# Kernel optimization log

Hardware: AMD Instinct MI355X
Metric: run time of the kernel (lower is better)

Reference implementation:

```python
import jax, jax.numpy as jnp
import numpy as np

K_CORR = 2048        # num_correspondences (init kwarg)
MAX_CORR = 8192      # static pad size for the variable-length nonzero output
THRES_START = 0.5
THRES_STEP = 0.01


def setup_inputs() -> dict:
    key = jax.random.key(0)
    k1, k2, k3 = jax.random.split(key, 3)
    N = M = 8193  # 8192 superpoints + 1 dustbin
    # shift so exp(scores) is mostly well below the 0.5 starting threshold,
    # making the iterative threshold search actually iterate (as in practice
    # with log-domain OT scores)
    matching_scores = jax.random.normal(k1, (N, M), dtype=jnp.float32) - 5.0
    ref_n2p_scores_c = jax.random.uniform(k2, (N - 1,), dtype=jnp.float32)
    src_n2p_scores_c = jax.random.uniform(k3, (M - 1,), dtype=jnp.float32)
    return {
        "matching_scores": matching_scores,
        "ref_n2p_scores_c": ref_n2p_scores_c,
        "src_n2p_scores_c": src_n2p_scores_c,
    }


def _find_thres(inner, k):
    """Replicates: while count(score[:-1,:-1] > thres) < k: thres -= 0.01."""
    def cond(t):
        return jnp.sum(inner > t) < k
    def body(t):
        return t - jnp.float32(THRES_STEP)
    return jax.lax.while_loop(cond, body, jnp.float32(THRES_START))


def reference(matching_scores, ref_n2p_scores_c, src_n2p_scores_c):
    s = jnp.exp(matching_scores)
    # n2p reweighting of the non-dustbin block, as in the torch in-place update
    inner = s[:-1, :-1] * (ref_n2p_scores_c[:, None] * src_n2p_scores_c[None, :])
    # threshold search is discrete -> not differentiated
    thres = _find_thres(jax.lax.stop_gradient(inner), K_CORR)
    mask = inner > thres
    count = jnp.sum(mask)
    # torch returns variable-length nonzero in row-major order; we pad to MAX_CORR
    r, c = jnp.nonzero(mask, size=MAX_CORR, fill_value=0)
    valid = jnp.arange(MAX_CORR) < count
    corr_scores = jnp.where(valid, inner[r, c], 0.0)
    ref_corr_indices = jnp.where(valid, r, -1)
    src_corr_indices = jnp.where(valid, c, -1)
    return ref_corr_indices, src_corr_indices, corr_scores
```

## Files before the change

### kernel.cpp

```cpp
#include <hip/hip_runtime.h>

#define NROWS 8192
#define NCOLS 8192
#define LD    8193
#define NBINS 64
#define KCORR 2048
#define MAXC  8192
#define CAP   192
#define RPB   4
#define FCUT_LOG (-2.5257286443082556f)

__device__ __forceinline__ float inner_val(float m, float rr, float sc) {
    float p = rr * sc;
    return expf(m) * p;
}

__global__ void init_kernel(float* __restrict__ out, unsigned* __restrict__ hist,
                            unsigned* __restrict__ ovfl) {
    int i = blockIdx.x * blockDim.x + threadIdx.x;
    if (i < 2 * MAXC)       out[i] = -1.0f;
    else if (i < 3 * MAXC)  out[i] = 0.0f;
    if (i < NBINS) hist[i] = 0u;
    if (i == NBINS) *ovfl = 0u;
}

__global__ __launch_bounds__(256) void hist_kernel(
    const float* __restrict__ ms, const float* __restrict__ refs,
    const float* __restrict__ srcs, unsigned* __restrict__ hist,
    unsigned* __restrict__ candcnt, unsigned* __restrict__ cand_col,
    float* __restrict__ cand_v, unsigned* __restrict__ ovfl, int use_cand)
{
    __shared__ float t[NBINS];
    __shared__ unsigned sub[NBINS];
    __shared__ unsigned cnt[RPB];
    __shared__ uint2 pairs[RPB * CAP];
    int tid = threadIdx.x;
    if (tid == 0) {
        float tv = 0.5f;
        for (int n = 0; n < NBINS; ++n) { t[n] = tv; tv = tv - 0.01f; }
    }
    if (tid < NBINS) sub[tid] = 0u;
    if (tid < RPB) cnt[tid] = 0u;
    __syncthreads();

    int r0 = blockIdx.x * RPB;

    auto push = [&](int r, int col, float m) {
        unsigned slot = atomicAdd(&cnt[r], 1u);
        if (slot < CAP)
            pairs[r * CAP + slot] = make_uint2((unsigned)col, __float_as_uint(m));
    };
    auto issue = [&](int b, float4* dst) {
        int r = b >> 1, h = b & 1;
        int row = r0 + r;
        int s = (4 - (row & 3)) & 3;
        const float4* p4 = (const float4*)(ms + (size_t)row * LD + s);
        int nb = (NCOLS - s) >> 2;
        #pragma unroll
        for (int k = 0; k < 4; ++k) {
            int i = h * 1024 + k * 256 + tid;
            if ((h == 1 && k == 3) ? (i < nb) : true) dst[k] = p4[i];
            else dst[k] = make_float4(-1e30f, -1e30f, -1e30f, -1e30f);
        }
    };
    auto consume = [&](int b, const float4* src4) {
        int r = b >> 1, h = b & 1;
        int s = (4 - ((r0 + r) & 3)) & 3;
        #pragma unroll
        for (int k = 0; k < 4; ++k) {
            float4 q = src4[k];
            int c0 = s + 4 * (h * 1024 + k * 256 + tid);
            bool a0 = q.x > FCUT_LOG, a1 = q.y > FCUT_LOG;
            bool a2 = q.z > FCUT_LOG, a3 = q.w > FCUT_LOG;
            if (a0 | a1 | a2 | a3) {
                if (a0) push(r, c0 + 0, q.x);
                if (a1) push(r, c0 + 1, q.y);
                if (a2) push(r, c0 + 2, q.z);
                if (a3) push(r, c0 + 3, q.w);
            }
        }
    };

    float4 buf[2][4];
    issue(0, buf[0]);
    #pragma unroll
    for (int b = 0; b < 2 * RPB; ++b) {
        if (b + 1 < 2 * RPB) issue(b + 1, buf[(b + 1) & 1]);
        consume(b, buf[b & 1]);
    }

    if (tid < RPB * 8) {
        int r = tid >> 3, e = tid & 7;
        int row = r0 + r;
        int s = (4 - (row & 3)) & 3;
        int nb = (NCOLS - s) >> 2;
        int done = s + 4 * nb;
        int col = -1;
        if (e < s) col = e;
        else if (e - s < NCOLS - done) col = done + (e - s);
        if (col >= 0) {
            float m = ms[(size_t)row * LD + col];
            if (m > FCUT_LOG) push(r, col, m);
        }
    }
    __syncthreads();

    for (int r = 0; r < RPB; ++r) {
        int row = r0 + r;
        unsigned C = cnt[r];
        unsigned Cc = (C < CAP) ? C : CAP;
        float rr = refs[row];
        for (unsigned i = tid; i < Cc; i += 256) {
            uint2 pr = pairs[r * CAP + i];
            int col = (int)pr.x;
            float m = __uint_as_float(pr.y);
            float v = inner_val(m, rr, srcs[col]);
            int g = (int)floorf((0.5f - v) * 100.0f) + 1;
            g = (g < 0) ? 0 : ((g > NBINS) ? NBINS : g);
            while (g < NBINS && t[g] >= v) ++g;
            while (g > 0 && t[g - 1] < v) --g;
            atomicAdd(&sub[g], 1u);
            if (use_cand) {
                cand_col[(size_t)row * CAP + i] = (unsigned)col;
                cand_v[(size_t)row * CAP + i]   = v;
            }
        }
        if (tid == 0) {
            if (use_cand) candcnt[row] = C;
            if (C > CAP) atomicOr(ovfl, 1u);
        }
    }
    __syncthreads();

    if (tid < 64) {
        unsigned v = sub[tid];
        unsigned p = v;
        #pragma unroll
        for (int off = 1; off < 64; off <<= 1) {
            unsigned u = __shfl_up(p, off);
            if (tid >= off) p += u;
        }
        unsigned binned = __shfl(p, 63);
        unsigned g = (tid == 63) ? (v + (unsigned)(RPB * NCOLS) - binned) : v;
        if (g) atomicAdd(&hist[tid], g);
    }
}

__global__ void mid_kernel(const unsigned* __restrict__ hist,
                           float* __restrict__ thres, unsigned* __restrict__ nstar) {
    int tid = threadIdx.x;
    if (tid < 64) {
        unsigned h = hist[tid];
        unsigned cum = h;
        #pragma unroll
        for (int off = 1; off < 64; off <<= 1) {
            unsigned u = __shfl_up(cum, off);
            if (tid >= off) cum += u;
        }
        unsigned long long mk = __ballot(cum >= (unsigned)KCORR);
        int nsel = mk ? (int)(__ffsll((unsigned long long)mk) - 1) : (NBINS - 1);
        if (tid == 0) {
            float tv = 0.5f;
            for (int n = 0; n < nsel; ++n) tv = tv - 0.01f;
            *thres = tv;
            *nstar = (unsigned)nsel;
        }
    }
}

__global__ __launch_bounds__(256) void rowcnt_kernel(
    const float* __restrict__ ms, const float* __restrict__ refs,
    const float* __restrict__ srcs, const float* __restrict__ thresp,
    const unsigned* __restrict__ nstar, const unsigned* __restrict__ ovfl,
    const unsigned* __restrict__ candcnt, const float* __restrict__ cand_v,
    unsigned* __restrict__ rowcnt, int use_cand)
{
    int ns = (int)*nstar;
    if (!(use_cand && ns <= 41 && *ovfl == 0u)) return;
    int tid = threadIdx.x, wv = tid >> 6, lane = tid & 63;
    int row = blockIdx.x * 4 + wv;
    float th = *thresp;
    unsigned C = candcnt[row];
    unsigned c = 0;
    if (C <= CAP) {
        const float* cv = cand_v + (size_t)row * CAP;
        for (unsigned i = lane; i < C; i += 64)
            c += (cv[i] > th) ? 1u : 0u;
    } else {
        float rr = refs[row];
        const float* mrow = ms + (size_t)row * LD;
        for (int col = lane; col < NCOLS; col += 64)
            c += (inner_val(mrow[col], rr, srcs[col]) > th) ? 1u : 0u;
    }
    #pragma unroll
    for (int off = 32; off > 0; off >>= 1) c += __shfl_down(c, off);
    if (lane == 0) rowcnt[row] = c;
}

__global__ __launch_bounds__(256) void count2_kernel(
    const float* __restrict__ ms, const float* __restrict__ refs,
    const float* __restrict__ srcs, const float* __restrict__ thresp,
    const unsigned* __restrict__ nstar, const unsigned* __restrict__ ovfl,
    unsigned* __restrict__ rowcnt, int use_cand)
{
    int ns = (int)*nstar;
    if (use_cand && ns <= 41 && *ovfl == 0u) return;
    __shared__ unsigned tot;
    float th = *thresp;
    for (int r4 = 0; r4 < 4; ++r4) {
        int row = blockIdx.x * 4 + r4;
        if (threadIdx.x == 0) tot = 0;
        __syncthreads();
        float rr = refs[row];
        const float* mrow = ms + (size_t)row * LD;
        unsigned c = 0;
        for (int col = threadIdx.x; col < NCOLS; col += 256)
            c += (inner_val(mrow[col], rr, srcs[col]) > th) ? 1u : 0u;
        atomicAdd(&tot, c);
        __syncthreads();
        if (threadIdx.x == 0) rowcnt[row] = tot;
        __syncthreads();
    }
}

__global__ __launch_bounds__(1024) void scan_kernel(
    const unsigned* __restrict__ rowcnt, unsigned* __restrict__ rowoff)
{
    __shared__ unsigned ssum[1024];
    int tid = threadIdx.x;
    int r0 = tid * 8;
    unsigned c[8], s = 0;
    #pragma unroll
    for (int k = 0; k < 8; ++k) { c[k] = rowcnt[r0 + k]; s += c[k]; }
    ssum[tid] = s;
    __syncthreads();
    for (int off = 1; off < 1024; off <<= 1) {
        unsigned v = (tid >= off) ? ssum[tid - off] : 0u;
        __syncthreads();
        ssum[tid] += v;
        __syncthreads();
    }
    unsigned excl = ssum[tid] - s;
    #pragma unroll
    for (int k = 0; k < 8; ++k) { rowoff[r0 + k] = excl; excl += c[k]; }
    if (tid == 1023) rowoff[NROWS] = excl;
}

__global__ __launch_bounds__(256) void cwrite_kernel(
    const float* __restrict__ ms, const float* __restrict__ refs,
    const float* __restrict__ srcs, const float* __restrict__ thresp,
    const unsigned* __restrict__ nstar, const unsigned* __restrict__ ovfl,
    const unsigned* __restrict__ rowoff, const unsigned* __restrict__ candcnt,
    const unsigned* __restrict__ cand_col, const float* __restrict__ cand_v,
    float* __restrict__ out, int use_cand)
{
    __shared__ unsigned s_col[4][64];
    __shared__ float    s_val[4][64];
    int tid = threadIdx.x, wv = tid >> 6, lane = tid & 63;
    int row = blockIdx.x * 4 + wv;
    unsigned base = rowoff[row], next = rowoff[row + 1];
    if (base == next || base >= MAXC) return;
    float th = *thresp;
    int ns = (int)*nstar;
    unsigned k = next - base;
    bool full = (!use_cand) || (ns >= 42) || (*ovfl != 0u) ||
                (candcnt[row] > CAP) || (k > 64);

    if (!full) {
        unsigned C = candcnt[row];
        const unsigned* cc = cand_col + (size_t)row * CAP;
        const float*    cv = cand_v  + (size_t)row * CAP;
        unsigned nrun = 0;
        for (unsigned c0 = 0; c0 < C; c0 += 64) {
            unsigned i = c0 + lane;
            bool sel = false; unsigned col = 0; float v = 0.f;
            if (i < C) { col = cc[i]; v = cv[i]; sel = (v > th); }
            unsigned long long mk = __ballot(sel);
            if (sel) {
                unsigned idx = nrun + (unsigned)__popcll(mk & ((1ull << lane) - 1ull));
                if (idx < 64) { s_col[wv][idx] = col; s_val[wv][idx] = v; }
            }
            nrun += (unsigned)__popcll(mk);
        }
        __builtin_amdgcn_s_waitcnt(0);
        __builtin_amdgcn_wave_barrier();
        unsigned kk = (nrun < k) ? nrun : k;
        if (kk > 64) kk = 64;
        if (lane < (int)kk) {
            unsigned mycol = s_col[wv][lane];
            float    myval = s_val[wv][lane];
            unsigned rank = 0;
            for (unsigned j = 0; j < kk; ++j)
                rank += (s_col[wv][j] < mycol) ? 1u : 0u;
            unsigned pos = base + rank;
            if (pos < MAXC) {
                out[pos]            = (float)row;
                out[MAXC + pos]     = (float)mycol;
                out[2 * MAXC + pos] = myval;
            }
        }
        return;
    }

    float rr = refs[row];
    const float* mrow = ms + (size_t)row * LD;
    unsigned running = base;
    for (int c0 = 0; c0 < NCOLS && running < next && running < MAXC; c0 += 64) {
        int col = c0 + lane;
        float v = inner_val(mrow[col], rr, srcs[col]);
        bool pred = v > th;
        unsigned long long mk = __ballot(pred);
        if (pred) {
            unsigned pos = running + (unsigned)__popcll(mk & ((1ull << lane) - 1ull));
            if (pos < MAXC) {
                out[pos]            = (float)row;
                out[MAXC + pos]     = (float)col;
                out[2 * MAXC + pos] = v;
            }
        }
        running += (unsigned)__popcll(mk);
    }
}

extern "C" void kernel_launch(void* const* d_in, const int* in_sizes, int n_in,
                              void* d_out, int out_size, void* d_ws, size_t ws_size,
                              hipStream_t stream) {
    const float* ms  = (const float*)d_in[0];
    const float* ref = (const float*)d_in[1];
    const float* src = (const float*)d_in[2];
    float* out = (float*)d_out;

    char* w = (char*)d_ws;
    unsigned* hist   = (unsigned*)(w);
    float*    thres  = (float*)(w + 256);
    unsigned* nstar  = (unsigned*)(w + 260);
    unsigned* ovfl   = (unsigned*)(w + 264);
    unsigned* rowcnt = (unsigned*)(w + 512);
    unsigned* rowoff = (unsigned*)(w + 512 + NROWS * 4);
    size_t cc_off = 512 + (size_t)NROWS * 4 + (size_t)(NROWS + 1) * 4;
    cc_off = (cc_off + 255) & ~(size_t)255;
    unsigned* candcnt  = (unsigned*)(w + cc_off);
    size_t col_off = cc_off + (size_t)NROWS * 4;
    unsigned* cand_col = (unsigned*)(w + col_off);
    size_t cv_off = col_off + (size_t)NROWS * CAP * 4;
    float* cand_v      = (float*)(w + cv_off);
    size_t end_off = cv_off + (size_t)NROWS * CAP * 4;

    int use_cand = (ws_size >= end_off) ? 1 : 0;

    init_kernel<<<96, 256, 0, stream>>>(out, hist, ovfl);
    hist_kernel<<<NROWS / RPB, 256, 0, stream>>>(ms, ref, src, hist, candcnt,
                                                 cand_col, cand_v, ovfl, use_cand);
    mid_kernel<<<1, 64, 0, stream>>>(hist, thres, nstar);
    rowcnt_kernel<<<NROWS / 4, 256, 0, stream>>>(ms, ref, src, thres, nstar,
                                                 ovfl, candcnt, cand_v, rowcnt,
                                                 use_cand);
    count2_kernel<<<NROWS / 4, 256, 0, stream>>>(ms, ref, src, thres, nstar,
                                                 ovfl, rowcnt, use_cand);
    scan_kernel<<<1, 1024, 0, stream>>>(rowcnt, rowoff);
    cwrite_kernel<<<NROWS / 4, 256, 0, stream>>>(ms, ref, src, thres, nstar,
                                                 ovfl, rowoff, candcnt, cand_col,
                                                 cand_v, out, use_cand);
}
```

Before: 382.7 us.

## Split histogram pass into flat mask scan plus sparse candidate expansion

Replaces the row-blocked histogram kernel with a flat, grid-strided float4 scan over the whole matrix. That scan emits 64-bit ballot masks of quads holding a value above the log cutoff. A second kernel expands only the flagged quads, bins them, and appends candidates per row with global atomics. A separate full-matrix histogram fallback (fb_hist plus mid2) runs only when the cutoff-based histogram cannot reach K. The aim is perfectly coalesced, alignment-free streaming of the large input and less per-row shared-memory work, at the cost of an extra mask buffer, global atomics on candcnt, and integer divisions to recover row and column.

Result: slower. 431.0 us (+12.6%).

```diff
diff --git a/kernel.cpp b/kernel.cpp
--- a/kernel.cpp
+++ b/kernel.cpp
@@ -2,181 +2,226 @@
 
 #define NROWS 8192
 #define NCOLS 8192
-#define LD    8193
+#define LDIM  8193
 #define NBINS 64
 #define KCORR 2048
 #define MAXC  8192
 #define CAP   192
-#define RPB   4
 #define FCUT_LOG (-2.5257286443082556f)
+
+#define NQUAD   16781312
+#define TILEQ   1024
+#define NTILES  16388
+#define NGROUPS 262208
 
 __device__ __forceinline__ float inner_val(float m, float rr, float sc) {
     float p = rr * sc;
     return expf(m) * p;
 }
 
+__device__ __forceinline__ void fold_thresholds(float* t) {
+    float tv = 0.5f;
+    for (int n = 0; n < NBINS; ++n) { t[n] = tv; tv = tv - 0.01f; }
+}
+
+__device__ __forceinline__ int exact_bin(float v, const float* t) {
+    int g = (int)floorf((0.5f - v) * 100.0f) + 1;
+    g = (g < 0) ? 0 : ((g > NBINS) ? NBINS : g);
+    while (g < NBINS && t[g] >= v) ++g;
+    while (g > 0 && t[g - 1] < v) --g;
+    return (g > 63) ? 63 : g;
+}
+
 __global__ void init_kernel(float* __restrict__ out, unsigned* __restrict__ hist,
-                            unsigned* __restrict__ ovfl) {
+                            unsigned* __restrict__ hist2,
+                            unsigned* __restrict__ candcnt,
+                            unsigned* __restrict__ fullmode) {
     int i = blockIdx.x * blockDim.x + threadIdx.x;
     if (i < 2 * MAXC)       out[i] = -1.0f;
     else if (i < 3 * MAXC)  out[i] = 0.0f;
-    if (i < NBINS) hist[i] = 0u;
-    if (i == NBINS) *ovfl = 0u;
-}
-
-__global__ __launch_bounds__(256) void hist_kernel(
+    if (i < NBINS) { hist[i] = 0u; hist2[i] = 0u; }
+    if (i == NBINS) *fullmode = 0u;
+    if (i < NROWS) candcnt[i] = 0u;
+}
+
+__global__ __launch_bounds__(256) void scan_mask_kernel(
+    const float* __restrict__ ms, unsigned long long* __restrict__ masks)
+{
+    const int tid = threadIdx.x;
+    const int lane = tid & 63, wv = tid >> 6;
+    const float4* m4 = (const float4*)ms;
+    const int g = gridDim.x;
+
+    float4 b0[4], b1[4];
+    auto issue = [&](int t, float4* B) {
+        const float4* p = m4 + (size_t)t * TILEQ + tid;
+        #pragma unroll
+        for (int k = 0; k < 4; ++k) B[k] = p[k * 256];
+    };
+    auto emit = [&](int t, const float4* B) {
+        unsigned long long mk0 = __ballot((B[0].x > FCUT_LOG) | (B[0].y > FCUT_LOG) |
+                                          (B[0].z > FCUT_LOG) | (B[0].w > FCUT_LOG));
+        unsigned long long mk1 = __ballot((B[1].x > FCUT_LOG) | (B[1].y > FCUT_LOG) |
+                                          (B[1].z > FCUT_LOG) | (B[1].w > FCUT_LOG));
+        unsigned long long mk2 = __ballot((B[2].x > FCUT_LOG) | (B[2].y > FCUT_LOG) |
+                                          (B[2].z > FCUT_LOG) | (B[2].w > FCUT_LOG));
+        unsigned long long mk3 = __ballot((B[3].x > FCUT_LOG) | (B[3].y > FCUT_LOG) |
+                                          (B[3].z > FCUT_LOG) | (B[3].w > FCUT_LOG));
+        unsigned long long val = (lane & 2) ? ((lane & 1) ? mk3 : mk2)
+                                            : ((lane & 1) ? mk1 : mk0);
+        if (lane < 4)
+            masks[(size_t)t * 16 + wv * 4 + lane] = val;
+    };
+
+    int t = blockIdx.x;
+    issue(t, b0);
+    while (true) {
+        int t1 = t + g;
+        if (t1 < NTILES) issue(t1, b1);
+        emit(t, b0);
+        t = t1;
+        if (t >= NTILES) break;
+        int t2 = t + g;
+        if (t2 < NTILES) issue(t2, b0);
+        emit(t, b1);
+        t = t2;
+        if (t >= NTILES) break;
+    }
+}
+
+__global__ __launch_bounds__(256) void expand_kernel(
     const float* __restrict__ ms, const float* __restrict__ refs,
-    const float* __restrict__ srcs, unsigned* __restrict__ hist,
-    unsigned* __restrict__ candcnt, unsigned* __restrict__ cand_col,
-    float* __restrict__ cand_v, unsigned* __restrict__ ovfl, int use_cand)
+    const float* __restrict__ srcs, const unsigned long long* __restrict__ masks,
+    unsigned* __restrict__ hist, unsigned* __restrict__ candcnt,
+    unsigned* __restrict__ cand_col, float* __restrict__ cand_v, int use_cand)
 {
     __shared__ float t[NBINS];
     __shared__ unsigned sub[NBINS];
-    __shared__ unsigned cnt[RPB];
-    __shared__ uint2 pairs[RPB * CAP];
     int tid = threadIdx.x;
+    if (tid == 0) fold_thresholds(t);
+    if (tid < NBINS) sub[tid] = 0u;
+    __syncthreads();
+
+    for (int i = blockIdx.x * 256 + tid; i < NGROUPS; i += gridDim.x * 256) {
+        unsigned long long mask = masks[i];
+        if (!mask) continue;
+        int tile = i >> 4, r = i & 15, w = r >> 2, k = r & 3;
+        int quadBase = tile * TILEQ + k * 256 + w * 64;
+        while (mask) {
+            int b = __ffsll((long long)mask) - 1;
+            mask &= mask - 1;
+            int q = quadBase + b;
+            float4 v4 = ((const float4*)ms)[q];
+            int e0 = q * 4;
+            #pragma unroll
+            for (int j = 0; j < 4; ++j) {
+                float m = (j == 0) ? v4.x : (j == 1) ? v4.y : (j == 2) ? v4.z : v4.w;
+                if (!(m > FCUT_LOG)) continue;
+                unsigned e = (unsigned)(e0 + j);
+                unsigned row = e / 8193u;
+                unsigned col = e - row * 8193u;
+                if (row >= NROWS || col >= NCOLS) continue;
+                float v = inner_val(m, refs[row], srcs[col]);
+                atomicAdd(&sub[exact_bin(v, t)], 1u);
+                if (use_cand) {
+                    unsigned slot = atomicAdd(&candcnt[row], 1u);
+                    if (slot < CAP) {
+                        cand_col[(size_t)row * CAP + slot] = col;
+                        cand_v[(size_t)row * CAP + slot]   = v;
+                    }
+                }
+            }
+        }
+    }
+    __syncthreads();
+    if (tid < NBINS && sub[tid]) atomicAdd(&hist[tid], sub[tid]);
+}
+
+__global__ void mid_kernel(const unsigned* __restrict__ hist,
+                           float* __restrict__ thres, unsigned* __restrict__ nstar,
+                           unsigned* __restrict__ fullmode) {
+    int tid = threadIdx.x;
+    unsigned cum = hist[tid];
+    #pragma unroll
+    for (int off = 1; off < 64; off <<= 1) {
+        unsigned u = __shfl_up(cum, off);
+        if (tid >= off) cum += u;
+    }
+    unsigned long long mk = __ballot(cum >= (unsigned)KCORR);
     if (tid == 0) {
-        float tv = 0.5f;
-        for (int n = 0; n < NBINS; ++n) { t[n] = tv; tv = tv - 0.01f; }
-    }
-    if (tid < NBINS) sub[tid] = 0u;
-    if (tid < RPB) cnt[tid] = 0u;
-    __syncthreads();
-
-    int r0 = blockIdx.x * RPB;
-
-    auto push = [&](int r, int col, float m) {
-        unsigned slot = atomicAdd(&cnt[r], 1u);
-        if (slot < CAP)
-            pairs[r * CAP + slot] = make_uint2((unsigned)col, __float_as_uint(m));
-    };
-    auto issue = [&](int b, float4* dst) {
-        int r = b >> 1, h = b & 1;
-        int row = r0 + r;
-        int s = (4 - (row & 3)) & 3;
-        const float4* p4 = (const float4*)(ms + (size_t)row * LD + s);
-        int nb = (NCOLS - s) >> 2;
-        #pragma unroll
-        for (int k = 0; k < 4; ++k) {
-            int i = h * 1024 + k * 256 + tid;
-            if ((h == 1 && k == 3) ? (i < nb) : true) dst[k] = p4[i];
-            else dst[k] = make_float4(-1e30f, -1e30f, -1e30f, -1e30f);
-        }
-    };
-    auto consume = [&](int b, const float4* src4) {
-        int r = b >> 1, h = b & 1;
-        int s = (4 - ((r0 + r) & 3)) & 3;
-        #pragma unroll
-        for (int k = 0; k < 4; ++k) {
-            float4 q = src4[k];
-            int c0 = s + 4 * (h * 1024 + k * 256 + tid);
-            bool a0 = q.x > FCUT_LOG, a1 = q.y > FCUT_LOG;
-            bool a2 = q.z > FCUT_LOG, a3 = q.w > FCUT_LOG;
-            if (a0 | a1 | a2 | a3) {
-                if (a0) push(r, c0 + 0, q.x);
-                if (a1) push(r, c0 + 1, q.y);
-                if (a2) push(r, c0 + 2, q.z);
-                if (a3) push(r, c0 + 3, q.w);
-            }
-        }
-    };
-
-    float4 buf[2][4];
-    issue(0, buf[0]);
-    #pragma unroll
-    for (int b = 0; b < 2 * RPB; ++b) {
-        if (b + 1 < 2 * RPB) issue(b + 1, buf[(b + 1) & 1]);
-        consume(b, buf[b & 1]);
-    }
-
-    if (tid < RPB * 8) {
-        int r = tid >> 3, e = tid & 7;
-        int row = r0 + r;
-        int s = (4 - (row & 3)) & 3;
-        int nb = (NCOLS - s) >> 2;
-        int done = s + 4 * nb;
-        int col = -1;
-        if (e < s) col = e;
-        else if (e - s < NCOLS - done) col = done + (e - s);
-        if (col >= 0) {
-            float m = ms[(size_t)row * LD + col];
-            if (m > FCUT_LOG) push(r, col, m);
-        }
-    }
-    __syncthreads();
-
-    for (int r = 0; r < RPB; ++r) {
-        int row = r0 + r;
-        unsigned C = cnt[r];
-        unsigned Cc = (C < CAP) ? C : CAP;
-        float rr = refs[row];
-        for (unsigned i = tid; i < Cc; i += 256) {
-            uint2 pr = pairs[r * CAP + i];
-            int col = (int)pr.x;
-            float m = __uint_as_float(pr.y);
-            float v = inner_val(m, rr, srcs[col]);
-            int g = (int)floorf((0.5f - v) * 100.0f) + 1;
-            g = (g < 0) ? 0 : ((g > NBINS) ? NBINS : g);
-            while (g < NBINS && t[g] >= v) ++g;
-            while (g > 0 && t[g - 1] < v) --g;
-            atomicAdd(&sub[g], 1u);
-            if (use_cand) {
-                cand_col[(size_t)row * CAP + i] = (unsigned)col;
-                cand_v[(size_t)row * CAP + i]   = v;
-            }
-        }
-        if (tid == 0) {
-            if (use_cand) candcnt[row] = C;
-            if (C > CAP) atomicOr(ovfl, 1u);
-        }
-    }
-    __syncthreads();
-
-    if (tid < 64) {
-        unsigned v = sub[tid];
-        unsigned p = v;
-        #pragma unroll
-        for (int off = 1; off < 64; off <<= 1) {
-            unsigned u = __shfl_up(p, off);
-            if (tid >= off) p += u;
-        }
-        unsigned binned = __shfl(p, 63);
-        unsigned g = (tid == 63) ? (v + (unsigned)(RPB * NCOLS) - binned) : v;
-        if (g) atomicAdd(&hist[tid], g);
-    }
-}
-
-__global__ void mid_kernel(const unsigned* __restrict__ hist,
-                           float* __restrict__ thres, unsigned* __restrict__ nstar) {
-    int tid = threadIdx.x;
-    if (tid < 64) {
-        unsigned h = hist[tid];
-        unsigned cum = h;
-        #pragma unroll
-        for (int off = 1; off < 64; off <<= 1) {
-            unsigned u = __shfl_up(cum, off);
-            if (tid >= off) cum += u;
-        }
-        unsigned long long mk = __ballot(cum >= (unsigned)KCORR);
-        int nsel = mk ? (int)(__ffsll((unsigned long long)mk) - 1) : (NBINS - 1);
-        if (tid == 0) {
+        int nsel = mk ? (int)(__ffsll((long long)mk) - 1) : NBINS;
+        if (nsel <= 41) {
             float tv = 0.5f;
             for (int n = 0; n < nsel; ++n) tv = tv - 0.01f;
-            *thres = tv;
-            *nstar = (unsigned)nsel;
-        }
+            *thres = tv; *nstar = (unsigned)nsel; *fullmode = 0u;
+        } else {
+            *fullmode = 1u; *nstar = 63u; *thres = -1e30f;
+        }
+    }
+}
+
+__global__ __launch_bounds__(256) void fb_hist_kernel(
+    const float* __restrict__ ms, const float* __restrict__ refs,
+    const float* __restrict__ srcs, const unsigned* __restrict__ fullmode,
+    unsigned* __restrict__ hist2)
+{
+    if (*fullmode == 0u) return;
+    __shared__ float t[NBINS];
+    __shared__ unsigned sub[64 * 65];
+    int tid = threadIdx.x, lane = tid & 63;
+    if (tid == 0) fold_thresholds(t);
+    for (int i = tid; i < 64 * 65; i += 256) sub[i] = 0u;
+    __syncthreads();
+    unsigned* mysub = sub + lane * 65;
+    for (int q = blockIdx.x * 256 + tid; q < NQUAD; q += gridDim.x * 256) {
+        float4 v4 = ((const float4*)ms)[q];
+        int e0 = q * 4;
+        #pragma unroll
+        for (int j = 0; j < 4; ++j) {
+            float m = (j == 0) ? v4.x : (j == 1) ? v4.y : (j == 2) ? v4.z : v4.w;
+            unsigned e = (unsigned)(e0 + j);
+            unsigned row = e / 8193u;
+            unsigned col = e - row * 8193u;
+            if (row >= NROWS || col >= NCOLS) continue;
+            float v = inner_val(m, refs[row], srcs[col]);
+            atomicAdd(&mysub[exact_bin(v, t)], 1u);
+        }
+    }
+    __syncthreads();
+    if (tid < 64) {
+        unsigned s = 0;
+        for (int c = 0; c < 64; ++c) s += sub[c * 65 + tid];
+        if (s) atomicAdd(&hist2[tid], s);
+    }
+}
+
+__global__ void mid2_kernel(const unsigned* __restrict__ hist2,
+                            const unsigned* __restrict__ fullmode,
+                            float* __restrict__ thres, unsigned* __restrict__ nstar) {
+    if (*fullmode == 0u) return;
+    int tid = threadIdx.x;
+    unsigned cum = hist2[tid];
+    #pragma unroll
+    for (int off = 1; off < 64; off <<= 1) {
+        unsigned u = __shfl_up(cum, off);
+        if (tid >= off) cum += u;
+    }
+    unsigned long long mk = __ballot(cum >= (unsigned)KCORR);
+    if (tid == 0) {
+        int nsel = mk ? (int)(__ffsll((long long)mk) - 1) : (NBINS - 1);
+        float tv = 0.5f;
+        for (int n = 0; n < nsel; ++n) tv = tv - 0.01f;
+        *thres = tv; *nstar = (unsigned)nsel;
     }
 }
 
 __global__ __launch_bounds__(256) void rowcnt_kernel(
     const float* __restrict__ ms, const float* __restrict__ refs,
     const float* __restrict__ srcs, const float* __restrict__ thresp,
-    const unsigned* __restrict__ nstar, const unsigned* __restrict__ ovfl,
-    const unsigned* __restrict__ candcnt, const float* __restrict__ cand_v,
-    unsigned* __restrict__ rowcnt, int use_cand)
-{
-    int ns = (int)*nstar;
-    if (!(use_cand && ns <= 41 && *ovfl == 0u)) return;
+    const unsigned* __restrict__ fullmode, const unsigned* __restrict__ candcnt,
+    const float* __restrict__ cand_v, unsigned* __restrict__ rowcnt, int use_cand)
+{
+    if (!use_cand || *fullmode != 0u) return;
     int tid = threadIdx.x, wv = tid >> 6, lane = tid & 63;
     int row = blockIdx.x * 4 + wv;
     float th = *thresp;
@@ -184,11 +229,10 @@
     unsigned c = 0;
     if (C <= CAP) {
         const float* cv = cand_v + (size_t)row * CAP;
-        for (unsigned i = lane; i < C; i += 64)
-            c += (cv[i] > th) ? 1u : 0u;
+        for (unsigned i = lane; i < C; i += 64) c += (cv[i] > th) ? 1u : 0u;
     } else {
         float rr = refs[row];
-        const float* mrow = ms + (size_t)row * LD;
+        const float* mrow = ms + (size_t)row * LDIM;
         for (int col = lane; col < NCOLS; col += 64)
             c += (inner_val(mrow[col], rr, srcs[col]) > th) ? 1u : 0u;
     }
@@ -200,11 +244,10 @@
 __global__ __launch_bounds__(256) void count2_kernel(
     const float* __restrict__ ms, const float* __restrict__ refs,
     const float* __restrict__ srcs, const float* __restrict__ thresp,
-    const unsigned* __restrict__ nstar, const unsigned* __restrict__ ovfl,
-    unsigned* __restrict__ rowcnt, int use_cand)
-{
-    int ns = (int)*nstar;
-    if (use_cand && ns <= 41 && *ovfl == 0u) return;
+    const unsigned* __restrict__ fullmode, unsigned* __restrict__ rowcnt,
+    int use_cand)
+{
+    if (use_cand && *fullmode == 0u) return;
     __shared__ unsigned tot;
     float th = *thresp;
     for (int r4 = 0; r4 < 4; ++r4) {
@@ -212,7 +255,7 @@
         if (threadIdx.x == 0) tot = 0;
         __syncthreads();
         float rr = refs[row];
-        const float* mrow = ms + (size_t)row * LD;
+        const float* mrow = ms + (size_t)row * LDIM;
         unsigned c = 0;
         for (int col = threadIdx.x; col < NCOLS; col += 256)
             c += (inner_val(mrow[col], rr, srcs[col]) > th) ? 1u : 0u;
@@ -249,10 +292,9 @@
 __global__ __launch_bounds__(256) void cwrite_kernel(
     const float* __restrict__ ms, const float* __restrict__ refs,
     const float* __restrict__ srcs, const float* __restrict__ thresp,
-    const unsigned* __restrict__ nstar, const unsigned* __restrict__ ovfl,
-    const unsigned* __restrict__ rowoff, const unsigned* __restrict__ candcnt,
-    const unsigned* __restrict__ cand_col, const float* __restrict__ cand_v,
-    float* __restrict__ out, int use_cand)
+    const unsigned* __restrict__ fullmode, const unsigned* __restrict__ rowoff,
+    const unsigned* __restrict__ candcnt, const unsigned* __restrict__ cand_col,
+    const float* __restrict__ cand_v, float* __restrict__ out, int use_cand)
 {
     __shared__ unsigned s_col[4][64];
     __shared__ float    s_val[4][64];
@@ -261,10 +303,8 @@
     unsigned base = rowoff[row], next = rowoff[row + 1];
     if (base == next || base >= MAXC) return;
     float th = *thresp;
-    int ns = (int)*nstar;
     unsigned k = next - base;
-    bool full = (!use_cand) || (ns >= 42) || (*ovfl != 0u) ||
-                (candcnt[row] > CAP) || (k > 64);
+    bool full = (!use_cand) || (*fullmode != 0u) || (candcnt[row] > CAP) || (k > 64);
 
     if (!full) {
         unsigned C = candcnt[row];
@@ -303,7 +343,7 @@
     }
 
     float rr = refs[row];
-    const float* mrow = ms + (size_t)row * LD;
+    const float* mrow = ms + (size_t)row * LDIM;
     unsigned running = base;
     for (int c0 = 0; c0 < NCOLS && running < next && running < MAXC; c0 += 64) {
         int col = c0 + lane;
@@ -331,34 +371,41 @@
     float* out = (float*)d_out;
 
     char* w = (char*)d_ws;
-    unsigned* hist   = (unsigned*)(w);
-    float*    thres  = (float*)(w + 256);
-    unsigned* nstar  = (unsigned*)(w + 260);
-    unsigned* ovfl   = (unsigned*)(w + 264);
-    unsigned* rowcnt = (unsigned*)(w + 512);
-    unsigned* rowoff = (unsigned*)(w + 512 + NROWS * 4);
-    size_t cc_off = 512 + (size_t)NROWS * 4 + (size_t)(NROWS + 1) * 4;
-    cc_off = (cc_off + 255) & ~(size_t)255;
-    unsigned* candcnt  = (unsigned*)(w + cc_off);
-    size_t col_off = cc_off + (size_t)NROWS * 4;
+    unsigned* hist     = (unsigned*)(w);
+    unsigned* hist2    = (unsigned*)(w + 256);
+    float*    thres    = (float*)(w + 512);
+    unsigned* nstar    = (unsigned*)(w + 516);
+    unsigned* fullmode = (unsigned*)(w + 520);
+    unsigned* rowcnt   = (unsigned*)(w + 1024);
+    unsigned* rowoff   = (unsigned*)(w + 1024 + NROWS * 4);
+    size_t cc_off = (1024 + (size_t)NROWS * 4 + (size_t)(NROWS + 1) * 4 + 255) & ~(size_t)255;
+    unsigned* candcnt = (unsigned*)(w + cc_off);
+    size_t mk_off  = cc_off + (size_t)NROWS * 4;
+    unsigned long long* masks = (unsigned long long*)(w + mk_off);
+    size_t col_off = mk_off + (size_t)NGROUPS * 8;
     unsigned* cand_col = (unsigned*)(w + col_off);
-    size_t cv_off = col_off + (size_t)NROWS * CAP * 4;
-    float* cand_v      = (float*)(w + cv_off);
+    size_t cv_off  = col_off + (size_t)NROWS * CAP * 4;
+    float* cand_v  = (float*)(w + cv_off);
     size_t end_off = cv_off + (size_t)NROWS * CAP * 4;
 
+    int use_mask = (ws_size >= col_off) ? 1 : 0;
     int use_cand = (ws_size >= end_off) ? 1 : 0;
 
-    init_kernel<<<96, 256, 0, stream>>>(out, hist, ovfl);
-    hist_kernel<<<NROWS / RPB, 256, 0, stream>>>(ms, ref, src, hist, candcnt,
-                                                 cand_col, cand_v, ovfl, use_cand);
-    mid_kernel<<<1, 64, 0, stream>>>(hist, thres, nstar);
-    rowcnt_kernel<<<NROWS / 4, 256, 0, stream>>>(ms, ref, src, thres, nstar,
-                                                 ovfl, candcnt, cand_v, rowcnt,
-                                                 use_cand);
-    count2_kernel<<<NROWS / 4, 256, 0, stream>>>(ms, ref, src, thres, nstar,
-                                                 ovfl, rowcnt, use_cand);
+    init_kernel<<<96, 256, 0, stream>>>(out, hist, hist2, candcnt, fullmode);
+    if (use_mask) {
+        scan_mask_kernel<<<2048, 256, 0, stream>>>(ms, masks);
+        expand_kernel<<<1024, 256, 0, stream>>>(ms, ref, src, masks, hist,
+                                                candcnt, cand_col, cand_v, use_cand);
+    }
+    mid_kernel<<<1, 64, 0, stream>>>(hist, thres, nstar, fullmode);
+    fb_hist_kernel<<<2048, 256, 0, stream>>>(ms, ref, src, fullmode, hist2);
+    mid2_kernel<<<1, 64, 0, stream>>>(hist2, fullmode, thres, nstar);
+    rowcnt_kernel<<<NROWS / 4, 256, 0, stream>>>(ms, ref, src, thres, fullmode,
+                                                 candcnt, cand_v, rowcnt, use_cand);
+    count2_kernel<<<NROWS / 4, 256, 0, stream>>>(ms, ref, src, thres, fullmode,
+                                                 rowcnt, use_cand);
     scan_kernel<<<1, 1024, 0, stream>>>(rowcnt, rowoff);
-    cwrite_kernel<<<NROWS / 4, 256, 0, stream>>>(ms, ref, src, thres, nstar,
-                                                 ovfl, rowoff, candcnt, cand_col,
+    cwrite_kernel<<<NROWS / 4, 256, 0, stream>>>(ms, ref, src, thres, fullmode,
+                                                 rowoff, candcnt, cand_col,
                                                  cand_v, out, use_cand);
 }
```
